# Kernel optimization log

Measured on AMD Instinct MI355X. Metric: run time of the kernel, lower is better.

The kernel has to match this reference:

```python
import jax, jax.numpy as jnp
import numpy as np

DEPTH = 3
DIM = 64
N_NODES = 4096
BATCH = 4


def setup_inputs() -> dict:
    key = jax.random.key(0)
    k1, k2, k3, k4 = jax.random.split(key, 4)
    x = jax.random.normal(k1, (BATCH, N_NODES, DIM), dtype=jnp.float32)
    graph = jax.random.uniform(k2, (BATCH, N_NODES, N_NODES), dtype=jnp.float32)
    # Linear((depth+1)*dim, dim): PyTorch default init U(-1/sqrt(fan_in), 1/sqrt(fan_in))
    fan_in = (DEPTH + 1) * DIM
    bound = 1.0 / np.sqrt(fan_in)
    W = jax.random.uniform(k3, (DIM, fan_in), minval=-bound, maxval=bound, dtype=jnp.float32)
    b = jax.random.uniform(k4, (DIM,), minval=-bound, maxval=bound, dtype=jnp.float32)
    return {"x": x, "graph": graph, "W": W, "b": b}


def reference(x, graph, W, b):
    # GCN branch of LocalGNN.forward (dropout p=0 -> identity).
    n = graph.shape[-1]
    g = graph + jnp.eye(n, dtype=graph.dtype)          # add self loops
    d = 1.0 / (jnp.sqrt(g.sum(axis=-1)) + 1e-7)        # [b, n]
    # D @ g @ D with D = diag(d):  g_ij * d_i * d_j
    g = g * d[..., :, None] * d[..., None, :]
    outs = [x]
    h = x
    for _ in range(DEPTH):
        h = jnp.einsum('bij,bjd->bid', g, h)           # dense propagation
        outs.append(h)
    cat = jnp.concatenate(outs, axis=-1)               # [b, n, (depth+1)*dim]
    return cat @ W.T + b
```

## Files before the change

### kernel.cpp

```cpp
#include <hip/hip_runtime.h>
#include <hip/hip_bf16.h>


typedef __attribute__((ext_vector_type(4))) float  floatx4;
typedef __attribute__((ext_vector_type(8))) short  short8;

#define NB 4
#define NN 4096
#define ND 64
#define HF_B 262144

__device__ __forceinline__ unsigned short f2bf_bits(float v) {
    __hip_bfloat16 b = __float2bfloat16(v);
    return *reinterpret_cast<unsigned short*>(&b);
}
__device__ __forceinline__ float bf2f(unsigned short u) {
    unsigned int x = ((unsigned int)u) << 16;
    return *reinterpret_cast<float*>(&x);
}
__device__ __forceinline__ short8 pack8p(const float* v) {
    short8 r;
#pragma unroll
    for (int j = 0; j < 8; ++j) r[j] = (short)f2bf_bits(v[j]);
    return r;
}

__global__ __launch_bounds__(256) void prep_graph(const float* __restrict__ g,
                                                  const float* __restrict__ x,
                                                  const float* __restrict__ W,
                                                  float* __restrict__ dinv,
                                                  unsigned short* __restrict__ gswz,
                                                  unsigned short* __restrict__ hF0,
                                                  unsigned short* __restrict__ Wf) {
    __shared__ float tile[16][516];
    __shared__ float dl[16];
    int tt = blockIdx.x;
    int b = tt >> 8, mt = tt & 255;
    int t = threadIdx.x;
    const float* grow = g + ((size_t)b * NN + mt * 16) * NN;
    size_t outbase = (size_t)tt * 128 * 512;
    float rs = 0.f;

    for (int s0 = 0; s0 < NN; s0 += 512) {
        __syncthreads();
#pragma unroll
        for (int it = 0; it < 8; ++it) {
            int f4 = it * 256 + t;
            int r = f4 >> 7, c4 = f4 & 127;
            floatx4 v = *reinterpret_cast<const floatx4*>(grow + (size_t)r * NN + s0 + c4 * 4);
            *reinterpret_cast<floatx4*>(&tile[r][c4 * 4]) = v;
        }
        __syncthreads();
        {
            int r = t >> 4, c0 = t & 15;
            float s = 0.f;
#pragma unroll
            for (int j2 = 0; j2 < 32; ++j2) s += tile[r][c0 + j2 * 16];
            rs += s;
        }
#pragma unroll
        for (int gg = 0; gg < 4; ++gg) {
            int gi = gg * 256 + t;
            int kcl = gi >> 6;
            int ln = gi & 63;
            int m = ln & 15, q = ln >> 4;
            int i_row = mt * 16 + m;
            int kbase = s0 + kcl * 32 + q * 8;
            float v[8];
#pragma unroll
            for (int j = 0; j < 8; ++j) {
                float xv = tile[m][kcl * 32 + q * 8 + j];
                if (kbase + j == i_row) xv += 1.0f;
                v[j] = xv;
            }
            *reinterpret_cast<short8*>(gswz + outbase + ((size_t)((s0 >> 5) + kcl)) * 512 + ln * 8) = pack8p(v);
        }
    }
#pragma unroll
    for (int off = 8; off > 0; off >>= 1) rs += __shfl_down(rs, off, 16);
    if ((t & 15) == 0) {
        int r = t >> 4;
        float d = 1.0f / (sqrtf(rs + 1.0f) + 1e-7f);
        dinv[b * NN + mt * 16 + r] = d;
        dl[r] = d;
    }
    __syncthreads();
    {
        const float* xp = x + ((size_t)b * NN + mt * 16) * ND;
#pragma unroll
        for (int e = 0; e < 4; ++e) {
            int idx = e * 256 + t;
            tile[idx >> 6][idx & 63] = xp[idx];
        }
    }
    __syncthreads();
    if (t < 128) {
        int c = t >> 5, lnl = t & 31;
        int q_loc = lnl >> 4, m = lnl & 15;
        int u = mt & 1;
        int ln = u * 32 + lnl;
        int kc = mt >> 1;
        float v[8];
#pragma unroll
        for (int j = 0; j < 8; ++j) {
            int lr = q_loc * 8 + j;
            v[j] = dl[lr] * tile[lr][c * 16 + m];
        }
        *reinterpret_cast<short8*>(hF0 + (size_t)b * HF_B + ((size_t)(kc * 4 + c) * 64 + ln) * 8) = pack8p(v);
    }
    if (tt == 0) {
#pragma unroll
        for (int e = 0; e < 8; ++e) {
            int wi = e * 256 + t;
            int kc = wi >> 8;
            int c = (wi >> 6) & 3;
            int ln = wi & 63;
            int m = ln & 15, q = ln >> 4;
            float v[8];
#pragma unroll
            for (int j = 0; j < 8; ++j) v[j] = W[(size_t)(c * 16 + m) * 256 + kc * 32 + q * 8 + j];
            *reinterpret_cast<short8*>(Wf + ((size_t)(kc * 4 + c) * 64 + ln) * 8) = pack8p(v);
        }
    }
}

#define PROP_MAIN()                                                                      \
    int bid = blockIdx.x;                                                                \
    int b = bid >> 7, mk = bid & 127;                                                    \
    int t = threadIdx.x;                                                                 \
    int w = t >> 6, lane = t & 63;                                                       \
    int m = lane & 15, q = lane >> 4;                                                    \
    int tt0 = b * 256 + mk * 2;                                                          \
    const unsigned short* Ap0 = gswz + ((size_t)tt0 * 128 + w * 32) * 512 + lane * 8;    \
    const unsigned short* Ap1 = Ap0 + (size_t)128 * 512;                                 \
    const unsigned short* Bp  = hFin + (size_t)b * HF_B + (size_t)(w * 32) * 2048 + lane * 8; \
    floatx4 acc0[4], acc1[4];                                                            \
    _Pragma("unroll")                                                                    \
    for (int c = 0; c < 4; ++c) { acc0[c] = (floatx4){0.f,0.f,0.f,0.f}; acc1[c] = acc0[c]; } \
    _Pragma("unroll 2")                                                                  \
    for (int kc = 0; kc < 32; ++kc) {                                                    \
        short8 a0 = *reinterpret_cast<const short8*>(Ap0);                               \
        short8 a1 = *reinterpret_cast<const short8*>(Ap1);                               \
        short8 b0 = *reinterpret_cast<const short8*>(Bp);                                \
        short8 b1 = *reinterpret_cast<const short8*>(Bp + 512);                          \
        short8 b2 = *reinterpret_cast<const short8*>(Bp + 1024);                         \
        short8 b3 = *reinterpret_cast<const short8*>(Bp + 1536);                         \
        Ap0 += 512; Ap1 += 512; Bp += 2048;                                              \
        acc0[0] = __builtin_amdgcn_mfma_f32_16x16x32_bf16(a0, b0, acc0[0], 0, 0, 0);     \
        acc1[0] = __builtin_amdgcn_mfma_f32_16x16x32_bf16(a1, b0, acc1[0], 0, 0, 0);     \
        acc0[1] = __builtin_amdgcn_mfma_f32_16x16x32_bf16(a0, b1, acc0[1], 0, 0, 0);     \
        acc1[1] = __builtin_amdgcn_mfma_f32_16x16x32_bf16(a1, b1, acc1[1], 0, 0, 0);     \
        acc0[2] = __builtin_amdgcn_mfma_f32_16x16x32_bf16(a0, b2, acc0[2], 0, 0, 0);     \
        acc1[2] = __builtin_amdgcn_mfma_f32_16x16x32_bf16(a1, b2, acc1[2], 0, 0, 0);     \
        acc0[3] = __builtin_amdgcn_mfma_f32_16x16x32_bf16(a0, b3, acc0[3], 0, 0, 0);     \
        acc1[3] = __builtin_amdgcn_mfma_f32_16x16x32_bf16(a1, b3, acc1[3], 0, 0, 0);     \
    }                                                                                    \
    if (t < 32) dl[t] = dinv[b * NN + mk * 32 + t];                                      \
    for (int u = 0; u < 2; ++u) {                                                        \
        __syncthreads();                                                                 \
        floatx4* acc = u ? acc1 : acc0;                                                  \
        _Pragma("unroll")                                                                \
        for (int c = 0; c < 4; ++c)                                                      \
            _Pragma("unroll")                                                            \
            for (int r = 0; r < 4; ++r) buf[w][q * 4 + r][c * 16 + m] = acc[c][r];       \
        __syncthreads();                                                                 \
        _Pragma("unroll")                                                                \
        for (int e = 0; e < 4; ++e) {                                                    \
            int idx = e * 256 + t;                                                       \
            int r = idx >> 6, col = idx & 63;                                            \
            float s = buf[0][r][col] + buf[1][r][col] + buf[2][r][col] + buf[3][r][col]; \
            int lr = u * 16 + r;                                                         \
            hsh[lr][col] = f2bf_bits(dl[lr] * s);                                        \
        }                                                                                \
    }                                                                                    \
    __syncthreads();

__global__ __launch_bounds__(256) void prop_pass(const unsigned short* __restrict__ gswz,
                                                 const unsigned short* __restrict__ hFin,
                                                 const float* __restrict__ dinv,
                                                 unsigned short* __restrict__ hrow,
                                                 unsigned short* __restrict__ hFout) {
    __shared__ float buf[4][16][68];
    __shared__ unsigned short hsh[32][64];
    __shared__ float dl[32];
    PROP_MAIN()
    {
        unsigned short* hp = hrow + ((size_t)b * NN + mk * 32) * ND;
#pragma unroll
        for (int e = 0; e < 8; ++e) {
            int idx = e * 256 + t;
            hp[idx] = hsh[idx >> 6][idx & 63];
        }
    }
    {
        int c = t >> 6, ln = t & 63;
        int mm = ln & 15, qq = ln >> 4;
        float v[8];
#pragma unroll
        for (int j = 0; j < 8; ++j) {
            int lr = qq * 8 + j;
            v[j] = dl[lr] * bf2f(hsh[lr][c * 16 + mm]);
        }
        *reinterpret_cast<short8*>(hFout + (size_t)b * HF_B + ((size_t)(mk * 4 + c) * 64 + ln) * 8) = pack8p(v);
    }
}

__global__ __launch_bounds__(256) void prop_final(const unsigned short* __restrict__ gswz,
                                                  const unsigned short* __restrict__ hFin,
                                                  const float* __restrict__ dinv,
                                                  const float* __restrict__ x,
                                                  const unsigned short* __restrict__ hrow1,
                                                  const unsigned short* __restrict__ hrow2,
                                                  const unsigned short* __restrict__ Wf,
                                                  const float* __restrict__ bias,
                                                  float* __restrict__ out) {
    __shared__ float buf[4][16][68];
    __shared__ unsigned short hsh[32][64];
    __shared__ float dl[32];
    PROP_MAIN()
    if (w < 2) {
        int u = w;
        int grow = b * NN + mk * 32 + u * 16 + m;
        floatx4 facc[4];
#pragma unroll
        for (int c = 0; c < 4; ++c) facc[c] = (floatx4){0.f, 0.f, 0.f, 0.f};
#pragma unroll
        for (int p = 0; p < 4; ++p) {
#pragma unroll
            for (int ki = 0; ki < 2; ++ki) {
                short8 af;
                if (p == 0) {
                    const float* xp = x + (size_t)grow * ND + ki * 32 + q * 8;
                    float v[8];
#pragma unroll
                    for (int j = 0; j < 8; ++j) v[j] = xp[j];
                    af = pack8p(v);
                } else if (p == 1) {
                    af = *reinterpret_cast<const short8*>(hrow1 + (size_t)grow * ND + ki * 32 + q * 8);
                } else if (p == 2) {
                    af = *reinterpret_cast<const short8*>(hrow2 + (size_t)grow * ND + ki * 32 + q * 8);
                } else {
                    af = *reinterpret_cast<const short8*>(&hsh[u * 16 + m][ki * 32 + q * 8]);
                }
                int kc = p * 2 + ki;
#pragma unroll
                for (int c = 0; c < 4; ++c) {
                    short8 bf = *reinterpret_cast<const short8*>(Wf + ((size_t)(kc * 4 + c) * 64 + lane) * 8);
                    facc[c] = __builtin_amdgcn_mfma_f32_16x16x32_bf16(af, bf, facc[c], 0, 0, 0);
                }
            }
        }
#pragma unroll
        for (int c = 0; c < 4; ++c) {
            float bb = bias[c * 16 + m];
#pragma unroll
            for (int r = 0; r < 4; ++r) {
                int row = b * NN + mk * 32 + u * 16 + q * 4 + r;
                out[(size_t)row * ND + c * 16 + m] = facc[c][r] + bb;
            }
        }
    }
}

extern "C" void kernel_launch(void* const* d_in, const int* in_sizes, int n_in,
                              void* d_out, int out_size, void* d_ws, size_t ws_size,
                              hipStream_t stream) {
    const float* x     = (const float*)d_in[0];
    const float* graph = (const float*)d_in[1];
    const float* W     = (const float*)d_in[2];
    const float* bias  = (const float*)d_in[3];
    float* out = (float*)d_out;

    char* w = (char*)d_ws;
    float*          dinv  = (float*)w;
    unsigned short* Wf    = (unsigned short*)(w + (1 << 16));
    unsigned short* hFa   = (unsigned short*)(w + (1 << 17));
    unsigned short* hFb   = hFa + (size_t)NB * HF_B;
    unsigned short* hrow1 = hFb + (size_t)NB * HF_B;
    unsigned short* hrow2 = hrow1 + (size_t)NB * NN * ND;
    unsigned short* gswz  = hrow2 + (size_t)NB * NN * ND;

    prep_graph<<<1024, 256, 0, stream>>>(graph, x, W, dinv, gswz, hFa, Wf);
    prop_pass<<<512, 256, 0, stream>>>(gswz, hFa, dinv, hrow1, hFb);
    prop_pass<<<512, 256, 0, stream>>>(gswz, hFb, dinv, hrow2, hFa);
    prop_final<<<512, 256, 0, stream>>>(gswz, hFa, dinv, x, hrow1, hrow2, Wf, bias, out);
}
```

Measured before the change: 496.7 us.

## Halve propagation row tile, prefetch operands, drop LDS staging in graph prep

The graph-prep kernel now loads rows directly into registers in the MFMA-swizzled order and reduces row sums with shuffles, removing the large LDS tile and its barriers. The propagation kernels shrink from 32 to 16 rows per block and double the grid to 1024 blocks, with software prefetch of the next A/B fragments. The final projection spreads output column groups across all four waves. Launch bounds request four blocks per CU. The aim is more parallelism and better latency hiding, at the cost of losing the A-reuse of two row tiles per B load, which doubles hF reads.

```diff
diff --git a/kernel.cpp b/kernel.cpp
--- a/kernel.cpp
+++ b/kernel.cpp
@@ -25,239 +25,206 @@
     return r;
 }
 
-__global__ __launch_bounds__(256) void prep_graph(const float* __restrict__ g,
-                                                  const float* __restrict__ x,
-                                                  const float* __restrict__ W,
-                                                  float* __restrict__ dinv,
-                                                  unsigned short* __restrict__ gswz,
-                                                  unsigned short* __restrict__ hF0,
-                                                  unsigned short* __restrict__ Wf) {
-    __shared__ float tile[16][516];
+__global__ __launch_bounds__(256, 4) void prep_graph(const float* __restrict__ g,
+                                                     const float* __restrict__ x,
+                                                     const float* __restrict__ W,
+                                                     float* __restrict__ dinv,
+                                                     unsigned short* __restrict__ gswz,
+                                                     unsigned short* __restrict__ hF0,
+                                                     unsigned short* __restrict__ Wf) {
+    __shared__ float rsum[4][16];
     __shared__ float dl[16];
     int tt = blockIdx.x;
     int b = tt >> 8, mt = tt & 255;
     int t = threadIdx.x;
-    const float* grow = g + ((size_t)b * NN + mt * 16) * NN;
+    int w = t >> 6, lane = t & 63;
+    int m = lane & 15, q = lane >> 4;
+    const float* rowp = g + ((size_t)b * NN + mt * 16 + m) * NN;
     size_t outbase = (size_t)tt * 128 * 512;
+    int i_row = mt * 16 + m;
     float rs = 0.f;
 
     for (int s0 = 0; s0 < NN; s0 += 512) {
-        __syncthreads();
-#pragma unroll
-        for (int it = 0; it < 8; ++it) {
-            int f4 = it * 256 + t;
-            int r = f4 >> 7, c4 = f4 & 127;
-            floatx4 v = *reinterpret_cast<const floatx4*>(grow + (size_t)r * NN + s0 + c4 * 4);
-            *reinterpret_cast<floatx4*>(&tile[r][c4 * 4]) = v;
-        }
-        __syncthreads();
-        {
-            int r = t >> 4, c0 = t & 15;
+#pragma unroll
+        for (int gg = 0; gg < 4; ++gg) {
+            int kcl = gg * 4 + w;
+            int kbase = s0 + kcl * 32 + q * 8;
+            floatx4 v0 = *reinterpret_cast<const floatx4*>(rowp + kbase);
+            floatx4 v1 = *reinterpret_cast<const floatx4*>(rowp + kbase + 4);
+            float v[8];
+#pragma unroll
+            for (int j = 0; j < 4; ++j) { v[j] = v0[j]; v[4 + j] = v1[j]; }
             float s = 0.f;
 #pragma unroll
-            for (int j2 = 0; j2 < 32; ++j2) s += tile[r][c0 + j2 * 16];
+            for (int j = 0; j < 8; ++j) s += v[j];
             rs += s;
-        }
-#pragma unroll
-        for (int gg = 0; gg < 4; ++gg) {
-            int gi = gg * 256 + t;
-            int kcl = gi >> 6;
-            int ln = gi & 63;
-            int m = ln & 15, q = ln >> 4;
-            int i_row = mt * 16 + m;
-            int kbase = s0 + kcl * 32 + q * 8;
-            float v[8];
-#pragma unroll
-            for (int j = 0; j < 8; ++j) {
-                float xv = tile[m][kcl * 32 + q * 8 + j];
-                if (kbase + j == i_row) xv += 1.0f;
-                v[j] = xv;
-            }
-            *reinterpret_cast<short8*>(gswz + outbase + ((size_t)((s0 >> 5) + kcl)) * 512 + ln * 8) = pack8p(v);
-        }
-    }
-#pragma unroll
-    for (int off = 8; off > 0; off >>= 1) rs += __shfl_down(rs, off, 16);
-    if ((t & 15) == 0) {
-        int r = t >> 4;
-        float d = 1.0f / (sqrtf(rs + 1.0f) + 1e-7f);
-        dinv[b * NN + mt * 16 + r] = d;
-        dl[r] = d;
-    }
+            int dj = i_row - kbase;
+            if (dj >= 0 && dj < 8) v[dj] += 1.0f;
+            *reinterpret_cast<short8*>(gswz + outbase + ((size_t)((s0 >> 5) + kcl)) * 512 + (size_t)lane * 8) = pack8p(v);
+        }
+    }
+    rs += __shfl_xor(rs, 16);
+    rs += __shfl_xor(rs, 32);
+    if (lane < 16) rsum[w][lane] = rs;
     __syncthreads();
-    {
-        const float* xp = x + ((size_t)b * NN + mt * 16) * ND;
-#pragma unroll
-        for (int e = 0; e < 4; ++e) {
-            int idx = e * 256 + t;
-            tile[idx >> 6][idx & 63] = xp[idx];
-        }
+    if (t < 16) {
+        float tot = rsum[0][t] + rsum[1][t] + rsum[2][t] + rsum[3][t];
+        float d = 1.0f / (sqrtf(tot + 1.0f) + 1e-7f);
+        dinv[b * NN + mt * 16 + t] = d;
+        dl[t] = d;
     }
     __syncthreads();
     if (t < 128) {
         int c = t >> 5, lnl = t & 31;
-        int q_loc = lnl >> 4, m = lnl & 15;
-        int u = mt & 1;
+        int q_loc = lnl >> 4, mm = lnl & 15;
+        int u = mt & 1, kc2 = mt >> 1;
         int ln = u * 32 + lnl;
-        int kc = mt >> 1;
+        const float* xp = x + ((size_t)b * NN + mt * 16) * ND + c * 16 + mm;
         float v[8];
 #pragma unroll
         for (int j = 0; j < 8; ++j) {
             int lr = q_loc * 8 + j;
-            v[j] = dl[lr] * tile[lr][c * 16 + m];
-        }
-        *reinterpret_cast<short8*>(hF0 + (size_t)b * HF_B + ((size_t)(kc * 4 + c) * 64 + ln) * 8) = pack8p(v);
+            v[j] = dl[lr] * xp[(size_t)lr * ND];
+        }
+        *reinterpret_cast<short8*>(hF0 + (size_t)b * HF_B + ((size_t)(kc2 * 4 + c) * 64 + ln) * 8) = pack8p(v);
     }
     if (tt == 0) {
 #pragma unroll
         for (int e = 0; e < 8; ++e) {
             int wi = e * 256 + t;
-            int kc = wi >> 8;
+            int kc2 = wi >> 8;
             int c = (wi >> 6) & 3;
             int ln = wi & 63;
-            int m = ln & 15, q = ln >> 4;
+            int mm = ln & 15, qq = ln >> 4;
             float v[8];
 #pragma unroll
-            for (int j = 0; j < 8; ++j) v[j] = W[(size_t)(c * 16 + m) * 256 + kc * 32 + q * 8 + j];
-            *reinterpret_cast<short8*>(Wf + ((size_t)(kc * 4 + c) * 64 + ln) * 8) = pack8p(v);
+            for (int j = 0; j < 8; ++j) v[j] = W[(size_t)(c * 16 + mm) * 256 + kc2 * 32 + qq * 8 + j];
+            *reinterpret_cast<short8*>(Wf + ((size_t)(kc2 * 4 + c) * 64 + ln) * 8) = pack8p(v);
         }
     }
 }
 
 #define PROP_MAIN()                                                                      \
     int bid = blockIdx.x;                                                                \
-    int b = bid >> 7, mk = bid & 127;                                                    \
+    int b = bid >> 8, mk = bid & 255;                                                    \
     int t = threadIdx.x;                                                                 \
     int w = t >> 6, lane = t & 63;                                                       \
     int m = lane & 15, q = lane >> 4;                                                    \
-    int tt0 = b * 256 + mk * 2;                                                          \
-    const unsigned short* Ap0 = gswz + ((size_t)tt0 * 128 + w * 32) * 512 + lane * 8;    \
-    const unsigned short* Ap1 = Ap0 + (size_t)128 * 512;                                 \
-    const unsigned short* Bp  = hFin + (size_t)b * HF_B + (size_t)(w * 32) * 2048 + lane * 8; \
-    floatx4 acc0[4], acc1[4];                                                            \
+    const unsigned short* Ap = gswz + ((size_t)(b * 256 + mk) * 128 + w * 32) * 512 + (size_t)lane * 8; \
+    const unsigned short* Bp = hFin + (size_t)b * HF_B + (size_t)(w * 32) * 2048 + (size_t)lane * 8;    \
+    floatx4 acc[4];                                                                      \
     _Pragma("unroll")                                                                    \
-    for (int c = 0; c < 4; ++c) { acc0[c] = (floatx4){0.f,0.f,0.f,0.f}; acc1[c] = acc0[c]; } \
+    for (int c = 0; c < 4; ++c) acc[c] = (floatx4){0.f, 0.f, 0.f, 0.f};                  \
+    short8 a_c  = *reinterpret_cast<const short8*>(Ap);                                  \
+    short8 b0_c = *reinterpret_cast<const short8*>(Bp);                                  \
+    short8 b1_c = *reinterpret_cast<const short8*>(Bp + 512);                            \
+    short8 b2_c = *reinterpret_cast<const short8*>(Bp + 1024);                           \
+    short8 b3_c = *reinterpret_cast<const short8*>(Bp + 1536);                           \
     _Pragma("unroll 2")                                                                  \
     for (int kc = 0; kc < 32; ++kc) {                                                    \
-        short8 a0 = *reinterpret_cast<const short8*>(Ap0);                               \
-        short8 a1 = *reinterpret_cast<const short8*>(Ap1);                               \
-        short8 b0 = *reinterpret_cast<const short8*>(Bp);                                \
-        short8 b1 = *reinterpret_cast<const short8*>(Bp + 512);                          \
-        short8 b2 = *reinterpret_cast<const short8*>(Bp + 1024);                         \
-        short8 b3 = *reinterpret_cast<const short8*>(Bp + 1536);                         \
-        Ap0 += 512; Ap1 += 512; Bp += 2048;                                              \
-        acc0[0] = __builtin_amdgcn_mfma_f32_16x16x32_bf16(a0, b0, acc0[0], 0, 0, 0);     \
-        acc1[0] = __builtin_amdgcn_mfma_f32_16x16x32_bf16(a1, b0, acc1[0], 0, 0, 0);     \
-        acc0[1] = __builtin_amdgcn_mfma_f32_16x16x32_bf16(a0, b1, acc0[1], 0, 0, 0);     \
-        acc1[1] = __builtin_amdgcn_mfma_f32_16x16x32_bf16(a1, b1, acc1[1], 0, 0, 0);     \
-        acc0[2] = __builtin_amdgcn_mfma_f32_16x16x32_bf16(a0, b2, acc0[2], 0, 0, 0);     \
-        acc1[2] = __builtin_amdgcn_mfma_f32_16x16x32_bf16(a1, b2, acc1[2], 0, 0, 0);     \
-        acc0[3] = __builtin_amdgcn_mfma_f32_16x16x32_bf16(a0, b3, acc0[3], 0, 0, 0);     \
-        acc1[3] = __builtin_amdgcn_mfma_f32_16x16x32_bf16(a1, b3, acc1[3], 0, 0, 0);     \
+        Ap += 512; Bp += 2048;                                                           \
+        short8 a_n  = *reinterpret_cast<const short8*>(Ap);                              \
+        short8 b0_n = *reinterpret_cast<const short8*>(Bp);                              \
+        short8 b1_n = *reinterpret_cast<const short8*>(Bp + 512);                        \
+        short8 b2_n = *reinterpret_cast<const short8*>(Bp + 1024);                       \
+        short8 b3_n = *reinterpret_cast<const short8*>(Bp + 1536);                       \
+        acc[0] = __builtin_amdgcn_mfma_f32_16x16x32_bf16(a_c, b0_c, acc[0], 0, 0, 0);    \
+        acc[1] = __builtin_amdgcn_mfma_f32_16x16x32_bf16(a_c, b1_c, acc[1], 0, 0, 0);    \
+        acc[2] = __builtin_amdgcn_mfma_f32_16x16x32_bf16(a_c, b2_c, acc[2], 0, 0, 0);    \
+        acc[3] = __builtin_amdgcn_mfma_f32_16x16x32_bf16(a_c, b3_c, acc[3], 0, 0, 0);    \
+        a_c = a_n; b0_c = b0_n; b1_c = b1_n; b2_c = b2_n; b3_c = b3_n;                   \
     }                                                                                    \
-    if (t < 32) dl[t] = dinv[b * NN + mk * 32 + t];                                      \
-    for (int u = 0; u < 2; ++u) {                                                        \
-        __syncthreads();                                                                 \
-        floatx4* acc = u ? acc1 : acc0;                                                  \
+    if (t < 16) dl[t] = dinv[b * NN + mk * 16 + t];                                      \
+    _Pragma("unroll")                                                                    \
+    for (int c = 0; c < 4; ++c)                                                          \
         _Pragma("unroll")                                                                \
-        for (int c = 0; c < 4; ++c)                                                      \
-            _Pragma("unroll")                                                            \
-            for (int r = 0; r < 4; ++r) buf[w][q * 4 + r][c * 16 + m] = acc[c][r];       \
-        __syncthreads();                                                                 \
-        _Pragma("unroll")                                                                \
-        for (int e = 0; e < 4; ++e) {                                                    \
-            int idx = e * 256 + t;                                                       \
-            int r = idx >> 6, col = idx & 63;                                            \
-            float s = buf[0][r][col] + buf[1][r][col] + buf[2][r][col] + buf[3][r][col]; \
-            int lr = u * 16 + r;                                                         \
-            hsh[lr][col] = f2bf_bits(dl[lr] * s);                                        \
-        }                                                                                \
+        for (int r = 0; r < 4; ++r) buf[w][q * 4 + r][c * 16 + m] = acc[c][r];           \
+    __syncthreads();                                                                     \
+    _Pragma("unroll")                                                                    \
+    for (int e = 0; e < 4; ++e) {                                                        \
+        int idx = e * 256 + t;                                                           \
+        int r = idx >> 6, col = idx & 63;                                                \
+        float s = buf[0][r][col] + buf[1][r][col] + buf[2][r][col] + buf[3][r][col];     \
+        hsh[r][col] = f2bf_bits(dl[r] * s);                                              \
     }                                                                                    \
     __syncthreads();
 
-__global__ __launch_bounds__(256) void prop_pass(const unsigned short* __restrict__ gswz,
-                                                 const unsigned short* __restrict__ hFin,
-                                                 const float* __restrict__ dinv,
-                                                 unsigned short* __restrict__ hrow,
-                                                 unsigned short* __restrict__ hFout) {
+__global__ __launch_bounds__(256, 4) void prop_pass(const unsigned short* __restrict__ gswz,
+                                                    const unsigned short* __restrict__ hFin,
+                                                    const float* __restrict__ dinv,
+                                                    unsigned short* __restrict__ hrow,
+                                                    unsigned short* __restrict__ hFout) {
     __shared__ float buf[4][16][68];
-    __shared__ unsigned short hsh[32][64];
-    __shared__ float dl[32];
+    __shared__ unsigned short hsh[16][64];
+    __shared__ float dl[16];
     PROP_MAIN()
     {
-        unsigned short* hp = hrow + ((size_t)b * NN + mk * 32) * ND;
-#pragma unroll
-        for (int e = 0; e < 8; ++e) {
+        unsigned short* hp = hrow + ((size_t)b * NN + mk * 16) * ND;
+#pragma unroll
+        for (int e = 0; e < 4; ++e) {
             int idx = e * 256 + t;
             hp[idx] = hsh[idx >> 6][idx & 63];
         }
     }
+    if (t < 128) {
+        int c = t >> 5, lnl = t & 31;
+        int q_loc = lnl >> 4, mm = lnl & 15;
+        int u = mk & 1, kc2 = mk >> 1;
+        int ln = u * 32 + lnl;
+        float v[8];
+#pragma unroll
+        for (int j = 0; j < 8; ++j) {
+            int lr = q_loc * 8 + j;
+            v[j] = dl[lr] * bf2f(hsh[lr][c * 16 + mm]);
+        }
+        *reinterpret_cast<short8*>(hFout + (size_t)b * HF_B + ((size_t)(kc2 * 4 + c) * 64 + ln) * 8) = pack8p(v);
+    }
+}
+
+__global__ __launch_bounds__(256, 4) void prop_final(const unsigned short* __restrict__ gswz,
+                                                     const unsigned short* __restrict__ hFin,
+                                                     const float* __restrict__ dinv,
+                                                     const float* __restrict__ x,
+                                                     const unsigned short* __restrict__ hrow1,
+                                                     const unsigned short* __restrict__ hrow2,
+                                                     const unsigned short* __restrict__ Wf,
+                                                     const float* __restrict__ bias,
+                                                     float* __restrict__ out) {
+    __shared__ float buf[4][16][68];
+    __shared__ unsigned short hsh[16][64];
+    __shared__ float dl[16];
+    PROP_MAIN()
     {
-        int c = t >> 6, ln = t & 63;
-        int mm = ln & 15, qq = ln >> 4;
-        float v[8];
-#pragma unroll
-        for (int j = 0; j < 8; ++j) {
-            int lr = qq * 8 + j;
-            v[j] = dl[lr] * bf2f(hsh[lr][c * 16 + mm]);
-        }
-        *reinterpret_cast<short8*>(hFout + (size_t)b * HF_B + ((size_t)(mk * 4 + c) * 64 + ln) * 8) = pack8p(v);
-    }
-}
-
-__global__ __launch_bounds__(256) void prop_final(const unsigned short* __restrict__ gswz,
-                                                  const unsigned short* __restrict__ hFin,
-                                                  const float* __restrict__ dinv,
-                                                  const float* __restrict__ x,
-                                                  const unsigned short* __restrict__ hrow1,
-                                                  const unsigned short* __restrict__ hrow2,
-                                                  const unsigned short* __restrict__ Wf,
-                                                  const float* __restrict__ bias,
-                                                  float* __restrict__ out) {
-    __shared__ float buf[4][16][68];
-    __shared__ unsigned short hsh[32][64];
-    __shared__ float dl[32];
-    PROP_MAIN()
-    if (w < 2) {
-        int u = w;
-        int grow = b * NN + mk * 32 + u * 16 + m;
-        floatx4 facc[4];
-#pragma unroll
-        for (int c = 0; c < 4; ++c) facc[c] = (floatx4){0.f, 0.f, 0.f, 0.f};
+        int grow_r = b * NN + mk * 16 + m;
+        floatx4 facc = (floatx4){0.f, 0.f, 0.f, 0.f};
 #pragma unroll
         for (int p = 0; p < 4; ++p) {
 #pragma unroll
             for (int ki = 0; ki < 2; ++ki) {
                 short8 af;
                 if (p == 0) {
-                    const float* xp = x + (size_t)grow * ND + ki * 32 + q * 8;
+                    const float* xp = x + (size_t)grow_r * ND + ki * 32 + q * 8;
                     float v[8];
 #pragma unroll
                     for (int j = 0; j < 8; ++j) v[j] = xp[j];
                     af = pack8p(v);
                 } else if (p == 1) {
-                    af = *reinterpret_cast<const short8*>(hrow1 + (size_t)grow * ND + ki * 32 + q * 8);
+                    af = *reinterpret_cast<const short8*>(hrow1 + (size_t)grow_r * ND + ki * 32 + q * 8);
                 } else if (p == 2) {
-                    af = *reinterpret_cast<const short8*>(hrow2 + (size_t)grow * ND + ki * 32 + q * 8);
+                    af = *reinterpret_cast<const short8*>(hrow2 + (size_t)grow_r * ND + ki * 32 + q * 8);
                 } else {
-                    af = *reinterpret_cast<const short8*>(&hsh[u * 16 + m][ki * 32 + q * 8]);
+                    af = *reinterpret_cast<const short8*>(&hsh[m][ki * 32 + q * 8]);
                 }
-                int kc = p * 2 + ki;
-#pragma unroll
-                for (int c = 0; c < 4; ++c) {
-                    short8 bf = *reinterpret_cast<const short8*>(Wf + ((size_t)(kc * 4 + c) * 64 + lane) * 8);
-                    facc[c] = __builtin_amdgcn_mfma_f32_16x16x32_bf16(af, bf, facc[c], 0, 0, 0);
-                }
+                int kc2 = p * 2 + ki;
+                short8 bf = *reinterpret_cast<const short8*>(Wf + ((size_t)(kc2 * 4 + w) * 64 + lane) * 8);
+                facc = __builtin_amdgcn_mfma_f32_16x16x32_bf16(af, bf, facc, 0, 0, 0);
             }
         }
-#pragma unroll
-        for (int c = 0; c < 4; ++c) {
-            float bb = bias[c * 16 + m];
-#pragma unroll
-            for (int r = 0; r < 4; ++r) {
-                int row = b * NN + mk * 32 + u * 16 + q * 4 + r;
-                out[(size_t)row * ND + c * 16 + m] = facc[c][r] + bb;
-            }
+        float bb = bias[w * 16 + m];
+#pragma unroll
+        for (int r = 0; r < 4; ++r) {
+            int row = b * NN + mk * 16 + q * 4 + r;
+            out[(size_t)row * ND + w * 16 + m] = facc[r] + bb;
         }
     }
 }
@@ -281,7 +248,7 @@
     unsigned short* gswz  = hrow2 + (size_t)NB * NN * ND;
 
     prep_graph<<<1024, 256, 0, stream>>>(graph, x, W, dinv, gswz, hFa, Wf);
-    prop_pass<<<512, 256, 0, stream>>>(gswz, hFa, dinv, hrow1, hFb);
-    prop_pass<<<512, 256, 0, stream>>>(gswz, hFb, dinv, hrow2, hFa);
-    prop_final<<<512, 256, 0, stream>>>(gswz, hFa, dinv, x, hrow1, hrow2, Wf, bias, out);
-}
+    prop_pass<<<1024, 256, 0, stream>>>(gswz, hFa, dinv, hrow1, hFb);
+    prop_pass<<<1024, 256, 0, stream>>>(gswz, hFb, dinv, hrow2, hFa);
+    prop_final<<<1024, 256, 0, stream>>>(gswz, hFa, dinv, x, hrow1, hrow2, Wf, bias, out);
+}
```

After: 485.8 us. 2.2% less time.
